# Kernel tuning notes

Hardware: AMD Instinct MI355X
Metric: run time of the kernel (lower is better)

The kernel has to match this reference:

```python
import jax, jax.numpy as jnp
import numpy as np
from jax import lax

B, H, W, L = 262144, 128, 16, 64

def setup_inputs() -> dict:
    key = jax.random.key(0)
    ks = jax.random.split(key, 6)
    scale = 1.0 / (0.1 + L * W)  # matches torch init scaling of program
    return {
        "x": jax.random.normal(ks[0], (B, H), dtype=jnp.float32),
        "program": jax.random.normal(ks[1], (L, W), dtype=jnp.float32) * scale,
        "wd": jax.random.normal(ks[2], (W, H), dtype=jnp.float32) * (1.0 / np.sqrt(H)),
        "bd": jax.random.normal(ks[3], (W,), dtype=jnp.float32) * 0.01,
        "wu": jax.random.normal(ks[4], (H, W), dtype=jnp.float32) * (1.0 / np.sqrt(W)),
        "bu": jax.random.normal(ks[5], (H,), dtype=jnp.float32) * 0.01,
    }

def reference(x, program, wd, bd, wu, bu):
    # Sequential processor loop: reg = relu(x @ wd.T + bd) * inst; x += reg @ wu.T + bu
    def step(xc, inst):
        reg = jax.nn.relu(xc @ wd.T + bd) * inst  # [B, W]
        xc = xc + reg @ wu.T + bu                  # [B, H]
        return xc, None
    x_out, _ = lax.scan(step, x, program)
    return x_out
```

## Files before the change

### kernel.cpp

```cpp
#include <hip/hip_runtime.h>

#define NB 262144
#define HH 128
#define WW 16
#define LL 64

typedef __attribute__((ext_vector_type(8))) short bf16x8;
typedef __attribute__((ext_vector_type(4))) float f32x4;
typedef __attribute__((ext_vector_type(2))) unsigned int u32x2;

union FragU { bf16x8 v; unsigned int u[4]; };

__device__ __forceinline__ unsigned int cvt_pk(float a, float b) {
    unsigned int r;
    asm("v_cvt_pk_bf16_f32 %0, %1, %2" : "=v"(r) : "v"(a), "v"(b));
    return r;
}

__global__ void kbu_kernel(const float* __restrict__ wd,
                           const float* __restrict__ bu,
                           float* __restrict__ kbu) {
    int c = threadIdx.x;
    if (c < WW) {
        float acc = 0.f;
        for (int h = 0; h < HH; ++h) acc = fmaf(wd[c * HH + h], bu[h], acc);
        kbu[c] = acc;
    }
}

__global__ __launch_bounds__(256, 4)
void proc_kernel(const float* __restrict__ x,
                 const float* __restrict__ program,
                 const float* __restrict__ wd,
                 const float* __restrict__ bd,
                 const float* __restrict__ wu,
                 const float* __restrict__ bu,
                 const float* __restrict__ kbu,
                 float* __restrict__ out)
{
    __shared__ __align__(16) float prog_lds[LL * WW];

    const int tid  = threadIdx.x;
    const int lane = tid & 63;
    const int wid  = tid >> 6;
    const int c    = lane & 15;
    const int q    = lane >> 4;
    const long row = (long)blockIdx.x * 64 + wid * 16 + c;

    {
        const float4* ps = (const float4*)program;
        float4* pd = (float4*)prog_lds;
        pd[tid] = ps[tid];
    }

    bf16x8 a_wd[4];
    #pragma unroll
    for (int kc = 0; kc < 4; ++kc) {
        const float* p = wd + c * HH + kc * 32 + q * 8;
        float4 f0 = *(const float4*)p;
        float4 f1 = *(const float4*)(p + 4);
        FragU u;
        u.u[0] = cvt_pk(f0.x, f0.y); u.u[1] = cvt_pk(f0.z, f0.w);
        u.u[2] = cvt_pk(f1.x, f1.y); u.u[3] = cvt_pk(f1.z, f1.w);
        a_wd[kc] = u.v;
    }

    bf16x8 a_wu[8];
    #pragma unroll
    for (int hc = 0; hc < 8; ++hc) {
        FragU u;
        if (q < 2) {
            const float* p = wu + (hc * 16 + c) * WW + q * 8;
            float4 f0 = *(const float4*)p;
            float4 f1 = *(const float4*)(p + 4);
            u.u[0] = cvt_pk(f0.x, f0.y); u.u[1] = cvt_pk(f0.z, f0.w);
            u.u[2] = cvt_pk(f1.x, f1.y); u.u[3] = cvt_pk(f1.z, f1.w);
        } else {
            u.u[0] = 0; u.u[1] = 0; u.u[2] = 0; u.u[3] = 0;
        }
        a_wu[hc] = u.v;
    }

    float4 bd4  = *(const float4*)(bd + q * 4);
    float4 kbu4 = *(const float4*)(kbu + q * 4);

    f32x4 acc[8];
    #pragma unroll
    for (int hc = 0; hc < 8; ++hc) {
        float4 f = *(const float4*)(x + row * HH + hc * 16 + q * 4);
        acc[hc][0] = f.x; acc[hc][1] = f.y; acc[hc][2] = f.z; acc[hc][3] = f.w;
    }

    __syncthreads();

    for (int l = 0; l < LL; ++l) {
        f32x4 dreg = {0.f, 0.f, 0.f, 0.f};
        #pragma unroll
        for (int kc = 0; kc < 4; ++kc) {
            unsigned a0 = cvt_pk(acc[2*kc  ][0], acc[2*kc  ][1]);
            unsigned a1 = cvt_pk(acc[2*kc  ][2], acc[2*kc  ][3]);
            unsigned b0 = cvt_pk(acc[2*kc+1][0], acc[2*kc+1][1]);
            unsigned b1 = cvt_pk(acc[2*kc+1][2], acc[2*kc+1][3]);
            u32x2 sa = __builtin_amdgcn_permlane32_swap(a0, b0, false, false);
            u32x2 ta = __builtin_amdgcn_permlane16_swap(sa[0], sa[1], false, false);
            u32x2 sb = __builtin_amdgcn_permlane32_swap(a1, b1, false, false);
            u32x2 tb = __builtin_amdgcn_permlane16_swap(sb[0], sb[1], false, false);
            FragU f;
            f.u[0] = ta[0]; f.u[1] = tb[0]; f.u[2] = ta[1]; f.u[3] = tb[1];
            dreg = __builtin_amdgcn_mfma_f32_16x16x32_bf16(a_wd[kc], f.v, dreg, 0, 0, 0);
        }

        float4 instv = *(const float4*)(&prog_lds[l * WW + q * 4]);
        float lf = (float)l;
        float r0 = fmaxf(dreg[0] + fmaf(lf, kbu4.x, bd4.x), 0.f) * instv.x;
        float r1 = fmaxf(dreg[1] + fmaf(lf, kbu4.y, bd4.y), 0.f) * instv.y;
        float r2 = fmaxf(dreg[2] + fmaf(lf, kbu4.z, bd4.z), 0.f) * instv.z;
        float r3 = fmaxf(dreg[3] + fmaf(lf, kbu4.w, bd4.w), 0.f) * instv.w;

        unsigned d0 = cvt_pk(r0, r1);
        unsigned d1 = cvt_pk(r2, r3);
        u32x2 s1 = __builtin_amdgcn_permlane32_swap(d0, d1, false, false);
        u32x2 t1 = __builtin_amdgcn_permlane16_swap(s1[0], s1[1], false, false);
        u32x2 g1 = __builtin_amdgcn_permlane32_swap(t1[0], t1[0], false, false);
        u32x2 g3 = __builtin_amdgcn_permlane32_swap(t1[1], t1[1], false, false);
        FragU rf;
        rf.u[0] = t1[0]; rf.u[1] = g1[1]; rf.u[2] = t1[1]; rf.u[3] = g3[1];

        #pragma unroll
        for (int hc = 0; hc < 8; ++hc) {
            acc[hc] = __builtin_amdgcn_mfma_f32_16x16x32_bf16(a_wu[hc], rf.v, acc[hc], 0, 0, 0);
        }
    }

    #pragma unroll
    for (int hc = 0; hc < 8; ++hc) {
        float4 bv = *(const float4*)(bu + hc * 16 + q * 4);
        float4 o;
        o.x = acc[hc][0] + 64.f * bv.x;
        o.y = acc[hc][1] + 64.f * bv.y;
        o.z = acc[hc][2] + 64.f * bv.z;
        o.w = acc[hc][3] + 64.f * bv.w;
        *(float4*)(out + row * HH + hc * 16 + q * 4) = o;
    }
}

extern "C" void kernel_launch(void* const* d_in, const int* in_sizes, int n_in,
                              void* d_out, int out_size, void* d_ws, size_t ws_size,
                              hipStream_t stream) {
    const float* x  = (const float*)d_in[0];
    const float* pr = (const float*)d_in[1];
    const float* wd = (const float*)d_in[2];
    const float* bd = (const float*)d_in[3];
    const float* wu = (const float*)d_in[4];
    const float* bu = (const float*)d_in[5];
    float* out = (float*)d_out;
    float* kbu = (float*)d_ws;

    kbu_kernel<<<1, 64, 0, stream>>>(wd, bu, kbu);
    proc_kernel<<<NB / 64, 256, 0, stream>>>(x, pr, wd, bd, wu, bu, kbu, out);
}
```

Baseline: 377.3 us.

## Permute weight fragment K-layout to eliminate cross-lane permlane swaps in loop

Measured after the change: 313.9 us. 1.2x faster.

```diff
diff --git a/kernel.cpp b/kernel.cpp
--- a/kernel.cpp
+++ b/kernel.cpp
@@ -7,7 +7,6 @@
 
 typedef __attribute__((ext_vector_type(8))) short bf16x8;
 typedef __attribute__((ext_vector_type(4))) float f32x4;
-typedef __attribute__((ext_vector_type(2))) unsigned int u32x2;
 
 union FragU { bf16x8 v; unsigned int u[4]; };
 
@@ -56,9 +55,9 @@
     bf16x8 a_wd[4];
     #pragma unroll
     for (int kc = 0; kc < 4; ++kc) {
-        const float* p = wd + c * HH + kc * 32 + q * 8;
+        const float* p = wd + c * HH + kc * 32 + q * 4;
         float4 f0 = *(const float4*)p;
-        float4 f1 = *(const float4*)(p + 4);
+        float4 f1 = *(const float4*)(p + 16);
         FragU u;
         u.u[0] = cvt_pk(f0.x, f0.y); u.u[1] = cvt_pk(f0.z, f0.w);
         u.u[2] = cvt_pk(f1.x, f1.y); u.u[3] = cvt_pk(f1.z, f1.w);
@@ -68,16 +67,11 @@
     bf16x8 a_wu[8];
     #pragma unroll
     for (int hc = 0; hc < 8; ++hc) {
+        const float* p = wu + (hc * 16 + c) * WW + q * 4;
+        float4 f0 = *(const float4*)p;
         FragU u;
-        if (q < 2) {
-            const float* p = wu + (hc * 16 + c) * WW + q * 8;
-            float4 f0 = *(const float4*)p;
-            float4 f1 = *(const float4*)(p + 4);
-            u.u[0] = cvt_pk(f0.x, f0.y); u.u[1] = cvt_pk(f0.z, f0.w);
-            u.u[2] = cvt_pk(f1.x, f1.y); u.u[3] = cvt_pk(f1.z, f1.w);
-        } else {
-            u.u[0] = 0; u.u[1] = 0; u.u[2] = 0; u.u[3] = 0;
-        }
+        u.u[0] = cvt_pk(f0.x, f0.y); u.u[1] = cvt_pk(f0.z, f0.w);
+        u.u[2] = 0; u.u[3] = 0;
         a_wu[hc] = u.v;
     }
 
@@ -93,43 +87,38 @@
 
     __syncthreads();
 
+    float lf = 0.f;
     for (int l = 0; l < LL; ++l) {
+        float4 instv = *(const float4*)(&prog_lds[l * WW + q * 4]);
+
         f32x4 dreg = {0.f, 0.f, 0.f, 0.f};
         #pragma unroll
         for (int kc = 0; kc < 4; ++kc) {
-            unsigned a0 = cvt_pk(acc[2*kc  ][0], acc[2*kc  ][1]);
-            unsigned a1 = cvt_pk(acc[2*kc  ][2], acc[2*kc  ][3]);
-            unsigned b0 = cvt_pk(acc[2*kc+1][0], acc[2*kc+1][1]);
-            unsigned b1 = cvt_pk(acc[2*kc+1][2], acc[2*kc+1][3]);
-            u32x2 sa = __builtin_amdgcn_permlane32_swap(a0, b0, false, false);
-            u32x2 ta = __builtin_amdgcn_permlane16_swap(sa[0], sa[1], false, false);
-            u32x2 sb = __builtin_amdgcn_permlane32_swap(a1, b1, false, false);
-            u32x2 tb = __builtin_amdgcn_permlane16_swap(sb[0], sb[1], false, false);
-            FragU f;
-            f.u[0] = ta[0]; f.u[1] = tb[0]; f.u[2] = ta[1]; f.u[3] = tb[1];
-            dreg = __builtin_amdgcn_mfma_f32_16x16x32_bf16(a_wd[kc], f.v, dreg, 0, 0, 0);
+            FragU b;
+            b.u[0] = cvt_pk(acc[2*kc  ][0], acc[2*kc  ][1]);
+            b.u[1] = cvt_pk(acc[2*kc  ][2], acc[2*kc  ][3]);
+            b.u[2] = cvt_pk(acc[2*kc+1][0], acc[2*kc+1][1]);
+            b.u[3] = cvt_pk(acc[2*kc+1][2], acc[2*kc+1][3]);
+            dreg = __builtin_amdgcn_mfma_f32_16x16x32_bf16(a_wd[kc], b.v, dreg, 0, 0, 0);
         }
 
-        float4 instv = *(const float4*)(&prog_lds[l * WW + q * 4]);
-        float lf = (float)l;
         float r0 = fmaxf(dreg[0] + fmaf(lf, kbu4.x, bd4.x), 0.f) * instv.x;
         float r1 = fmaxf(dreg[1] + fmaf(lf, kbu4.y, bd4.y), 0.f) * instv.y;
         float r2 = fmaxf(dreg[2] + fmaf(lf, kbu4.z, bd4.z), 0.f) * instv.z;
         float r3 = fmaxf(dreg[3] + fmaf(lf, kbu4.w, bd4.w), 0.f) * instv.w;
 
-        unsigned d0 = cvt_pk(r0, r1);
-        unsigned d1 = cvt_pk(r2, r3);
-        u32x2 s1 = __builtin_amdgcn_permlane32_swap(d0, d1, false, false);
-        u32x2 t1 = __builtin_amdgcn_permlane16_swap(s1[0], s1[1], false, false);
-        u32x2 g1 = __builtin_amdgcn_permlane32_swap(t1[0], t1[0], false, false);
-        u32x2 g3 = __builtin_amdgcn_permlane32_swap(t1[1], t1[1], false, false);
         FragU rf;
-        rf.u[0] = t1[0]; rf.u[1] = g1[1]; rf.u[2] = t1[1]; rf.u[3] = g3[1];
+        rf.u[0] = cvt_pk(r0, r1);
+        rf.u[1] = cvt_pk(r2, r3);
+        rf.u[2] = rf.u[0];
+        rf.u[3] = rf.u[1];
 
         #pragma unroll
         for (int hc = 0; hc < 8; ++hc) {
             acc[hc] = __builtin_amdgcn_mfma_f32_16x16x32_bf16(a_wu[hc], rf.v, acc[hc], 0, 0, 0);
         }
+
+        lf += 1.0f;
     }
 
     #pragma unroll
```
